# Performance work log

Measured on AMD Instinct MI355X. Metric: run time of the kernel, lower is better.

Reference implementation:

```python
import jax, jax.numpy as jnp
import numpy as np

IN_DIM = 128
OUT_DIM = 128
NUM_HEADS = 4
HEAD_DIM = OUT_DIM // NUM_HEADS
TEMP = 0.2
NEG_SLOPE = 0.2


def _xavier(key, shape, gain=1.414):
    fan_in, fan_out = shape[-2], shape[-1]
    limit = gain * np.sqrt(6.0 / (fan_in + fan_out))
    return jax.random.uniform(key, shape, jnp.float32, -limit, limit)


def setup_inputs() -> dict:
    key = jax.random.key(0)
    k_h, k_W, k_a, k_mw, k_mb = jax.random.split(key, 5)
    B, N = 4, 2048
    h = jax.random.normal(k_h, (B, N, IN_DIM), jnp.float32)
    W = _xavier(k_W, (NUM_HEADS, IN_DIM, HEAD_DIM))
    a = _xavier(k_a, (NUM_HEADS, 2 * HEAD_DIM, 1))
    merge_w = _xavier(k_mw, (OUT_DIM, OUT_DIM))  # nn.Linear weight [out, in]
    merge_b = jnp.zeros((OUT_DIM,), jnp.float32)
    return {"h": h, "W": W, "a": a, "merge_w": merge_w, "merge_b": merge_b}


def reference(h, W, a, merge_w, merge_b):
    B, N, _ = h.shape
    # Wh: [B, H, N, head_dim]
    Wh = jnp.einsum('bni,hio->bhno', h, W)
    a_sq = a[..., 0]                                  # [H, 2*hd]
    a_src, a_dst = a_sq[:, :HEAD_DIM], a_sq[:, HEAD_DIM:]
    # additive score decomposition avoids the NxNx2hd concat blowup
    s_src = jnp.einsum('bhno,ho->bhn', Wh, a_src)     # contribution of node i (row)
    s_dst = jnp.einsum('bhno,ho->bhn', Wh, a_dst)     # contribution of node j (col)
    e = s_src[:, :, :, None] + s_dst[:, :, None, :]   # [B, H, N, N]
    e = jnp.where(e > 0, e, NEG_SLOPE * e)            # LeakyReLU(0.2)
    alpha = jax.nn.softmax(e / TEMP, axis=3)          # softmax over neighbors j
    h_prime_heads = jnp.einsum('bhnm,bhmo->bhno', alpha, Wh)
    h_concat = h_prime_heads.transpose(0, 2, 1, 3).reshape(B, N, OUT_DIM)
    h_prime = h_concat @ merge_w.T + merge_b
    return h_prime, alpha.mean(axis=1)
```

## Files before the change

kernel.cpp:

```cpp
#include <hip/hip_runtime.h>
#include <stddef.h>

#define NN 2048
#define DIN 128
#define HD 32

typedef __attribute__((ext_vector_type(8))) short short8;
typedef __attribute__((ext_vector_type(4))) float f32x4;

constexpr float SLOPE = 0.2f;
constexpr float LC = 7.2134752044448170f;

__device__ __forceinline__ unsigned int pack_rne(float a, float b){
    unsigned int xa = __float_as_uint(a), xb = __float_as_uint(b);
    unsigned int ra = (xa + 0x7fffu + ((xa >> 16) & 1u)) >> 16;
    unsigned int rb = (xb + 0x7fffu + ((xb >> 16) & 1u)) >> 16;
    return ra | (rb << 16);
}

__global__ __launch_bounds__(256) void kWh(const float* __restrict__ hg,
                                           const float* __restrict__ Wg,
                                           float* __restrict__ Wh)
{
    __shared__ float Wl[DIN*HD];
    __shared__ float Hl[8][DIN+4];
    const int t = threadIdx.x;
    const int bh = blockIdx.x >> 5;
    const int tile = blockIdx.x & 31;
    const int b = bh >> 2, hh = bh & 3;
    for (int i = t; i < DIN*HD; i += 256) Wl[i] = Wg[hh*DIN*HD + i];
    const int o = t & 31, r = t >> 5;
    for (int it = 0; it < 8; ++it){
        const int nb = tile*64 + it*8;
        __syncthreads();
        {
            const float4 v = *(const float4*)&hg[((size_t)b*NN + nb + r)*DIN + o*4];
            *(float4*)&Hl[r][o*4] = v;
        }
        __syncthreads();
        float acc = 0.f;
        #pragma unroll 8
        for (int i = 0; i < DIN; ++i) acc = fmaf(Hl[r][i], Wl[i*HD+o], acc);
        Wh[((size_t)bh*NN + nb + r)*HD + o] = acc;
    }
}

__global__ __launch_bounds__(256) void kScore(const float* __restrict__ Wh,
                                              const float* __restrict__ ag,
                                              float* __restrict__ sSrc,
                                              float* __restrict__ sDst,
                                              float* __restrict__ maxPart)
{
    __shared__ float al[64];
    __shared__ float wred[4];
    const int t = threadIdx.x;
    const int bh = blockIdx.x >> 3, seg = blockIdx.x & 7;
    const int hh = bh & 3;
    if (t < 64) al[t] = ag[hh*64 + t];
    __syncthreads();
    const int n = seg*256 + t;
    const float4* wr = (const float4*)&Wh[((size_t)bh*NN + n)*HD];
    float ss = 0.f, sd = 0.f;
    #pragma unroll
    for (int q = 0; q < 8; ++q){
        float4 w = wr[q];
        ss += w.x*al[q*4+0] + w.y*al[q*4+1] + w.z*al[q*4+2] + w.w*al[q*4+3];
        sd += w.x*al[32+q*4+0] + w.y*al[32+q*4+1] + w.z*al[32+q*4+2] + w.w*al[32+q*4+3];
    }
    sSrc[bh*NN+n] = ss; sDst[bh*NN+n] = sd;
    float lmax = sd;
    #pragma unroll
    for (int off = 32; off > 0; off >>= 1) lmax = fmaxf(lmax, __shfl_down(lmax, off));
    if ((t & 63) == 0) wred[t >> 6] = lmax;
    __syncthreads();
    if (t == 0) maxPart[bh*8 + seg] = fmaxf(fmaxf(wred[0], wred[1]), fmaxf(wred[2], wred[3]));
}

__global__ __launch_bounds__(256) void kAttnM(const float* __restrict__ Wh,
                                              const float* __restrict__ sSrc,
                                              const float* __restrict__ sDst,
                                              const float* __restrict__ maxPart,
                                              float* __restrict__ invZ,
                                              unsigned short* __restrict__ hcb)
{
    __shared__ unsigned short WtT[32][136];
    __shared__ float sdl[128];
    const int t = threadIdx.x;
    const int wv = t >> 6, lane = t & 63;
    const int q = lane >> 4, c = lane & 15;
    const int bh = blockIdx.x >> 5;
    const int n0 = (blockIdx.x & 31)*64 + wv*16;
    const int b = bh >> 2, hh = bh & 3;
    float mx = maxPart[bh*8];
    #pragma unroll
    for (int i = 1; i < 8; ++i) mx = fmaxf(mx, maxPart[bh*8 + i]);
    const float ssrc = sSrc[bh*NN + n0 + c];
    const float q0 = ssrc + mx;
    const float R = fmaxf(q0, SLOPE*q0) * LC;
    const float a1 = ssrc*LC - R;
    const float a2 = SLOPE*LC*ssrc - R;
    f32x4 acc0 = {0.f,0.f,0.f,0.f}, acc1 = {0.f,0.f,0.f,0.f};
    float Zp = 0.f;
    const size_t whbase = (size_t)bh*NN*HD;
    for (int mt = 0; mt < 16; ++mt){
        const int mb = mt*128;
        __syncthreads();
        #pragma unroll
        for (int ii = 0; ii < 2; ++ii){
            const int idx = t + 256*ii;
            const int c4 = idx & 7, rp = idx >> 3;
            const float4 v0 = *(const float4*)&Wh[whbase + (size_t)(mb + 2*rp)*HD + c4*4];
            const float4 v1 = *(const float4*)&Wh[whbase + (size_t)(mb + 2*rp + 1)*HD + c4*4];
            const unsigned int* b0 = (const unsigned int*)&v0;
            const unsigned int* b1 = (const unsigned int*)&v1;
            #pragma unroll
            for (int k = 0; k < 4; ++k){
                unsigned int xa = b0[k], xb = b1[k];
                unsigned int pk = ((xa + 0x7fffu + ((xa>>16)&1u)) >> 16)
                                | (((xb + 0x7fffu + ((xb>>16)&1u)) >> 16) << 16);
                *(unsigned int*)&WtT[c4*4 + k][2*rp] = pk;
            }
        }
        if (t < 128) sdl[t] = LC * sDst[bh*NN + mb + t];
        __syncthreads();
        #pragma unroll
        for (int ks = 0; ks < 4; ++ks){
            const int m8 = ks*32 + q*8;
            float p[8];
            #pragma unroll
            for (int j = 0; j < 8; ++j){
                const float u = sdl[m8 + j];
                p[j] = exp2f(fmaxf(a1 + u, fmaf(SLOPE, u, a2)));
                Zp += p[j];
            }
            short8 aF;
            #pragma unroll
            for (int j = 0; j < 8; j += 2){
                ((unsigned int*)&aF)[j>>1] = (__float_as_uint(p[j]) >> 16)
                                           | (__float_as_uint(p[j+1]) & 0xffff0000u);
            }
            const short8 bF0 = *(const short8*)&WtT[c][m8];
            const short8 bF1 = *(const short8*)&WtT[16 + c][m8];
            acc0 = __builtin_amdgcn_mfma_f32_16x16x32_bf16(aF, bF0, acc0, 0, 0, 0);
            acc1 = __builtin_amdgcn_mfma_f32_16x16x32_bf16(aF, bF1, acc1, 0, 0, 0);
        }
    }
    Zp += __shfl_xor(Zp, 16);
    Zp += __shfl_xor(Zp, 32);
    const float iz = 1.0f / Zp;
    if (q == 0) invZ[bh*NN + n0 + c] = iz;
    #pragma unroll
    for (int reg = 0; reg < 4; ++reg){
        const int row = q*4 + reg;
        const float izr = __shfl(iz, row);
        const size_t base = ((size_t)b*NN + n0 + row)*128 + hh*32;
        hcb[base + c]      = (unsigned short)((pack_rne(acc0[reg]*izr, 0.f)) & 0xffffu);
        hcb[base + 16 + c] = (unsigned short)((pack_rne(acc1[reg]*izr, 0.f)) & 0xffffu);
    }
}

__global__ __launch_bounds__(256) void kAlpha(const float* __restrict__ sSrc,
                                              const float* __restrict__ sDst,
                                              const float* __restrict__ maxPart,
                                              const float* __restrict__ invZ,
                                              float* __restrict__ out1)
{
    __shared__ float sdl[4][NN];
    const int t = threadIdx.x;
    const int b = blockIdx.x >> 9;
    const int n0 = (blockIdx.x & 511) * 4;
    for (int i = t; i < 4*NN; i += 256)
        sdl[i >> 11][i & (NN-1)] = LC * sDst[(size_t)(b*4 + (i>>11))*NN + (i & (NN-1))];
    __syncthreads();
    float a1[4][4], a2[4][4], cf[4][4];
    #pragma unroll
    for (int hh = 0; hh < 4; ++hh){
        float mx = maxPart[(b*4+hh)*8];
        #pragma unroll
        for (int i = 1; i < 8; ++i) mx = fmaxf(mx, maxPart[(b*4+hh)*8 + i]);
        #pragma unroll
        for (int rr = 0; rr < 4; ++rr){
            const int bhn = (b*4+hh)*NN + n0 + rr;
            const float ss = sSrc[bhn];
            const float q0 = ss + mx;
            const float R = fmaxf(q0, SLOPE*q0)*LC;
            a1[rr][hh] = ss*LC - R;
            a2[rr][hh] = SLOPE*LC*ss - R;
            cf[rr][hh] = 0.25f * invZ[bhn];
        }
    }
    for (int mb = 0; mb < NN; mb += 256){
        const int m = mb + t;
        const float u0 = sdl[0][m], u1 = sdl[1][m], u2 = sdl[2][m], u3 = sdl[3][m];
        #pragma unroll
        for (int rr = 0; rr < 4; ++rr){
            float v;
            v  = cf[rr][0]*exp2f(fmaxf(a1[rr][0]+u0, fmaf(SLOPE, u0, a2[rr][0])));
            v += cf[rr][1]*exp2f(fmaxf(a1[rr][1]+u1, fmaf(SLOPE, u1, a2[rr][1])));
            v += cf[rr][2]*exp2f(fmaxf(a1[rr][2]+u2, fmaf(SLOPE, u2, a2[rr][2])));
            v += cf[rr][3]*exp2f(fmaxf(a1[rr][3]+u3, fmaf(SLOPE, u3, a2[rr][3])));
            out1[((size_t)b*NN + n0 + rr)*NN + m] = v;
        }
    }
}

__global__ __launch_bounds__(256) void kMergeM(const unsigned short* __restrict__ hcb,
                                               const float* __restrict__ mw,
                                               const float* __restrict__ mbv,
                                               float* __restrict__ out0)
{
    __shared__ unsigned short mwb[128][136];
    const int t = threadIdx.x;
    const int wv = t >> 6, lane = t & 63;
    const int q = lane >> 4, c = lane & 15;
    for (int i = t; i < 128*64; i += 256){
        const int j = i >> 6, k2 = i & 63;
        const float2 v = *(const float2*)&mw[j*128 + k2*2];
        *(unsigned int*)&mwb[j][k2*2] = pack_rne(v.x, v.y);
    }
    __syncthreads();
    const int row0 = blockIdx.x*64 + wv*16;
    f32x4 acc[8];
    #pragma unroll
    for (int ot = 0; ot < 8; ++ot) acc[ot] = (f32x4){0.f,0.f,0.f,0.f};
    #pragma unroll
    for (int ks = 0; ks < 4; ++ks){
        const short8 aF = *(const short8*)&hcb[((size_t)row0 + c)*128 + ks*32 + q*8];
        #pragma unroll
        for (int ot = 0; ot < 8; ++ot){
            const short8 bF = *(const short8*)&mwb[ot*16 + c][ks*32 + q*8];
            acc[ot] = __builtin_amdgcn_mfma_f32_16x16x32_bf16(aF, bF, acc[ot], 0, 0, 0);
        }
    }
    #pragma unroll
    for (int ot = 0; ot < 8; ++ot){
        const int col = ot*16 + c;
        const float bias = mbv[col];
        #pragma unroll
        for (int reg = 0; reg < 4; ++reg){
            const size_t row = (size_t)row0 + q*4 + reg;
            out0[row*128 + col] = acc[ot][reg] + bias;
        }
    }
}

extern "C" void kernel_launch(void* const* d_in, const int* in_sizes, int n_in,
                              void* d_out, int out_size, void* d_ws, size_t ws_size,
                              hipStream_t stream)
{
    const float* hg  = (const float*)d_in[0];
    const float* Wg  = (const float*)d_in[1];
    const float* ag  = (const float*)d_in[2];
    const float* mw  = (const float*)d_in[3];
    const float* mbv = (const float*)d_in[4];
    float* out0 = (float*)d_out;
    float* out1 = out0 + (size_t)4*NN*128;

    float* ws     = (float*)d_ws;
    float* Wh     = ws;
    float* sSrc   = Wh + 1048576;
    float* sDst   = sSrc + 32768;
    float* maxPart= sDst + 32768;
    float* invZ   = maxPart + 128;
    unsigned short* hcb = (unsigned short*)(invZ + 32768);

    hipLaunchKernelGGL(kWh,    dim3(512),  dim3(256), 0, stream, hg, Wg, Wh);
    hipLaunchKernelGGL(kScore, dim3(128),  dim3(256), 0, stream, Wh, ag, sSrc, sDst, maxPart);
    hipLaunchKernelGGL(kAttnM, dim3(512),  dim3(256), 0, stream, Wh, sSrc, sDst, maxPart, invZ, hcb);
    hipLaunchKernelGGL(kAlpha, dim3(2048), dim3(256), 0, stream, sSrc, sDst, maxPart, invZ, out1);
    hipLaunchKernelGGL(kMergeM,dim3(128),  dim3(256), 0, stream, hcb, mw, mbv, out0);
}
```

Measured before the change: 169.3 us.

## Fuse Wh projection with score computation and emit transposed bf16 Wh

```diff
diff --git a/kernel.cpp b/kernel.cpp
--- a/kernel.cpp
+++ b/kernel.cpp
@@ -18,68 +18,110 @@
     return ra | (rb << 16);
 }
 
-__global__ __launch_bounds__(256) void kWh(const float* __restrict__ hg,
-                                           const float* __restrict__ Wg,
-                                           float* __restrict__ Wh)
-{
-    __shared__ float Wl[DIN*HD];
-    __shared__ float Hl[8][DIN+4];
-    const int t = threadIdx.x;
-    const int bh = blockIdx.x >> 5;
-    const int tile = blockIdx.x & 31;
-    const int b = bh >> 2, hh = bh & 3;
-    for (int i = t; i < DIN*HD; i += 256) Wl[i] = Wg[hh*DIN*HD + i];
-    const int o = t & 31, r = t >> 5;
-    for (int it = 0; it < 8; ++it){
-        const int nb = tile*64 + it*8;
-        __syncthreads();
-        {
-            const float4 v = *(const float4*)&hg[((size_t)b*NN + nb + r)*DIN + o*4];
-            *(float4*)&Hl[r][o*4] = v;
-        }
-        __syncthreads();
-        float acc = 0.f;
-        #pragma unroll 8
-        for (int i = 0; i < DIN; ++i) acc = fmaf(Hl[r][i], Wl[i*HD+o], acc);
-        Wh[((size_t)bh*NN + nb + r)*HD + o] = acc;
-    }
-}
-
-__global__ __launch_bounds__(256) void kScore(const float* __restrict__ Wh,
-                                              const float* __restrict__ ag,
-                                              float* __restrict__ sSrc,
-                                              float* __restrict__ sDst,
-                                              float* __restrict__ maxPart)
-{
-    __shared__ float al[64];
-    __shared__ float wred[4];
-    const int t = threadIdx.x;
-    const int bh = blockIdx.x >> 3, seg = blockIdx.x & 7;
-    const int hh = bh & 3;
-    if (t < 64) al[t] = ag[hh*64 + t];
+__global__ __launch_bounds__(256) void kWhScore(const float* __restrict__ hg,
+                                                const float* __restrict__ Wg,
+                                                const float* __restrict__ ag,
+                                                unsigned short* __restrict__ whT,
+                                                float* __restrict__ sSrc,
+                                                float* __restrict__ sDst,
+                                                float* __restrict__ maxPart)
+{
+    __shared__ float Hl[32][132];
+    __shared__ float wal[8][128];
+    __shared__ float al[256];
+    const int t = threadIdx.x;
+    const int b = blockIdx.x >> 6;
+    const int tile = blockIdx.x & 63;
+    const int n0 = tile*32;
+    #pragma unroll
+    for (int ii = 0; ii < 4; ++ii){
+        const int idx = t + 256*ii;
+        const int r = idx >> 5, c4 = idx & 31;
+        *(float4*)&Hl[r][c4*4] = *(const float4*)&hg[((size_t)b*NN + n0 + r)*DIN + c4*4];
+    }
+    al[t] = ag[t];
     __syncthreads();
-    const int n = seg*256 + t;
-    const float4* wr = (const float4*)&Wh[((size_t)bh*NN + n)*HD];
-    float ss = 0.f, sd = 0.f;
-    #pragma unroll
-    for (int q = 0; q < 8; ++q){
-        float4 w = wr[q];
-        ss += w.x*al[q*4+0] + w.y*al[q*4+1] + w.z*al[q*4+2] + w.w*al[q*4+3];
-        sd += w.x*al[32+q*4+0] + w.y*al[32+q*4+1] + w.z*al[32+q*4+2] + w.w*al[32+q*4+3];
-    }
-    sSrc[bh*NN+n] = ss; sDst[bh*NN+n] = sd;
-    float lmax = sd;
-    #pragma unroll
-    for (int off = 32; off > 0; off >>= 1) lmax = fmaxf(lmax, __shfl_down(lmax, off));
-    if ((t & 63) == 0) wred[t >> 6] = lmax;
+    #pragma unroll
+    for (int jj = 0; jj < 4; ++jj){
+        const int idx = t + 256*jj;
+        const int combo = idx >> 7, i = idx & 127;
+        const int hh = combo >> 1, d = combo & 1;
+        const float* wrow = &Wg[hh*4096 + i*32];
+        const float* av = &al[hh*64 + d*32];
+        float s = 0.f;
+        #pragma unroll
+        for (int q = 0; q < 8; ++q){
+            const float4 w = *(const float4*)&wrow[q*4];
+            s += w.x*av[q*4] + w.y*av[q*4+1] + w.z*av[q*4+2] + w.w*av[q*4+3];
+        }
+        wal[combo][i] = s;
+    }
     __syncthreads();
-    if (t == 0) maxPart[bh*8 + seg] = fmaxf(fmaxf(wred[0], wred[1]), fmaxf(wred[2], wred[3]));
-}
-
-__global__ __launch_bounds__(256) void kAttnM(const float* __restrict__ Wh,
+    {
+        const int combo = t >> 5, nl = t & 31;
+        const int hh = combo >> 1, d = combo & 1;
+        float s = 0.f;
+        #pragma unroll
+        for (int q = 0; q < 32; ++q){
+            const float4 hv = *(const float4*)&Hl[nl][q*4];
+            const float4 wv = *(const float4*)&wal[combo][q*4];
+            s += hv.x*wv.x + hv.y*wv.y + hv.z*wv.z + hv.w*wv.w;
+        }
+        const int bh = b*4 + hh;
+        if (d == 0) sSrc[bh*NN + n0 + nl] = s;
+        else {
+            sDst[bh*NN + n0 + nl] = s;
+            float lm = s;
+            #pragma unroll
+            for (int off = 1; off < 32; off <<= 1) lm = fmaxf(lm, __shfl_xor(lm, off));
+            if (nl == 0) maxPart[bh*64 + tile] = lm;
+        }
+    }
+    const int og = t >> 5, nl = t & 31;
+    const int o0 = og*4;
+    float acc[16];
+    #pragma unroll
+    for (int k = 0; k < 16; ++k) acc[k] = 0.f;
+    for (int kc = 0; kc < 16; ++kc){
+        const float4 hA = *(const float4*)&Hl[nl][kc*8];
+        const float4 hB = *(const float4*)&Hl[nl][kc*8+4];
+        const float hreg[8] = {hA.x,hA.y,hA.z,hA.w,hB.x,hB.y,hB.z,hB.w};
+        #pragma unroll
+        for (int hh = 0; hh < 4; ++hh){
+            #pragma unroll
+            for (int i8 = 0; i8 < 8; ++i8){
+                const float4 w = *(const float4*)&Wg[hh*4096 + (kc*8+i8)*32 + o0];
+                acc[hh*4+0] = fmaf(hreg[i8], w.x, acc[hh*4+0]);
+                acc[hh*4+1] = fmaf(hreg[i8], w.y, acc[hh*4+1]);
+                acc[hh*4+2] = fmaf(hreg[i8], w.z, acc[hh*4+2]);
+                acc[hh*4+3] = fmaf(hreg[i8], w.w, acc[hh*4+3]);
+            }
+        }
+    }
+    #pragma unroll
+    for (int hh = 0; hh < 4; ++hh){
+        #pragma unroll
+        for (int j = 0; j < 4; ++j){
+            const unsigned int x = __float_as_uint(acc[hh*4+j]);
+            whT[((size_t)(b*4+hh)*32 + o0 + j)*NN + n0 + nl] =
+                (unsigned short)((x + 0x7fffu + ((x>>16)&1u)) >> 16);
+        }
+    }
+}
+
+__global__ void kMaxR(const float* __restrict__ maxPart, float* __restrict__ maxFull){
+    const int t = threadIdx.x;
+    if (t < 16){
+        float m = maxPart[t*64];
+        for (int i = 1; i < 64; ++i) m = fmaxf(m, maxPart[t*64+i]);
+        maxFull[t] = m;
+    }
+}
+
+__global__ __launch_bounds__(256) void kAttnM(const unsigned short* __restrict__ whT,
                                               const float* __restrict__ sSrc,
                                               const float* __restrict__ sDst,
-                                              const float* __restrict__ maxPart,
+                                              const float* __restrict__ maxFull,
                                               float* __restrict__ invZ,
                                               unsigned short* __restrict__ hcb)
 {
@@ -91,9 +133,7 @@
     const int bh = blockIdx.x >> 5;
     const int n0 = (blockIdx.x & 31)*64 + wv*16;
     const int b = bh >> 2, hh = bh & 3;
-    float mx = maxPart[bh*8];
-    #pragma unroll
-    for (int i = 1; i < 8; ++i) mx = fmaxf(mx, maxPart[bh*8 + i]);
+    const float mx = maxFull[bh];
     const float ssrc = sSrc[bh*NN + n0 + c];
     const float q0 = ssrc + mx;
     const float R = fmaxf(q0, SLOPE*q0) * LC;
@@ -101,25 +141,14 @@
     const float a2 = SLOPE*LC*ssrc - R;
     f32x4 acc0 = {0.f,0.f,0.f,0.f}, acc1 = {0.f,0.f,0.f,0.f};
     float Zp = 0.f;
-    const size_t whbase = (size_t)bh*NN*HD;
     for (int mt = 0; mt < 16; ++mt){
         const int mb = mt*128;
         __syncthreads();
         #pragma unroll
-        for (int ii = 0; ii < 2; ++ii){
-            const int idx = t + 256*ii;
-            const int c4 = idx & 7, rp = idx >> 3;
-            const float4 v0 = *(const float4*)&Wh[whbase + (size_t)(mb + 2*rp)*HD + c4*4];
-            const float4 v1 = *(const float4*)&Wh[whbase + (size_t)(mb + 2*rp + 1)*HD + c4*4];
-            const unsigned int* b0 = (const unsigned int*)&v0;
-            const unsigned int* b1 = (const unsigned int*)&v1;
-            #pragma unroll
-            for (int k = 0; k < 4; ++k){
-                unsigned int xa = b0[k], xb = b1[k];
-                unsigned int pk = ((xa + 0x7fffu + ((xa>>16)&1u)) >> 16)
-                                | (((xb + 0x7fffu + ((xb>>16)&1u)) >> 16) << 16);
-                *(unsigned int*)&WtT[c4*4 + k][2*rp] = pk;
-            }
+        for (int ps = 0; ps < 2; ++ps){
+            const int o = ps*16 + (t >> 4);
+            const int mo = (t & 15)*8;
+            *(short8*)&WtT[o][mo] = *(const short8*)&whT[((size_t)bh*32 + o)*NN + mb + mo];
         }
         if (t < 128) sdl[t] = LC * sDst[bh*NN + mb + t];
         __syncthreads();
@@ -161,7 +190,7 @@
 
 __global__ __launch_bounds__(256) void kAlpha(const float* __restrict__ sSrc,
                                               const float* __restrict__ sDst,
-                                              const float* __restrict__ maxPart,
+                                              const float* __restrict__ maxFull,
                                               const float* __restrict__ invZ,
                                               float* __restrict__ out1)
 {
@@ -175,9 +204,7 @@
     float a1[4][4], a2[4][4], cf[4][4];
     #pragma unroll
     for (int hh = 0; hh < 4; ++hh){
-        float mx = maxPart[(b*4+hh)*8];
-        #pragma unroll
-        for (int i = 1; i < 8; ++i) mx = fmaxf(mx, maxPart[(b*4+hh)*8 + i]);
+        const float mx = maxFull[b*4+hh];
         #pragma unroll
         for (int rr = 0; rr < 4; ++rr){
             const int bhn = (b*4+hh)*NN + n0 + rr;
@@ -256,17 +283,18 @@
     float* out0 = (float*)d_out;
     float* out1 = out0 + (size_t)4*NN*128;
 
-    float* ws     = (float*)d_ws;
-    float* Wh     = ws;
-    float* sSrc   = Wh + 1048576;
-    float* sDst   = sSrc + 32768;
-    float* maxPart= sDst + 32768;
-    float* invZ   = maxPart + 128;
-    unsigned short* hcb = (unsigned short*)(invZ + 32768);
-
-    hipLaunchKernelGGL(kWh,    dim3(512),  dim3(256), 0, stream, hg, Wg, Wh);
-    hipLaunchKernelGGL(kScore, dim3(128),  dim3(256), 0, stream, Wh, ag, sSrc, sDst, maxPart);
-    hipLaunchKernelGGL(kAttnM, dim3(512),  dim3(256), 0, stream, Wh, sSrc, sDst, maxPart, invZ, hcb);
-    hipLaunchKernelGGL(kAlpha, dim3(2048), dim3(256), 0, stream, sSrc, sDst, maxPart, invZ, out1);
-    hipLaunchKernelGGL(kMergeM,dim3(128),  dim3(256), 0, stream, hcb, mw, mbv, out0);
-}
+    float* ws      = (float*)d_ws;
+    float* sSrc    = ws;
+    float* sDst    = sSrc + 32768;
+    float* maxPart = sDst + 32768;
+    float* maxFull = maxPart + 1024;
+    float* invZ    = maxFull + 16;
+    unsigned short* whT = (unsigned short*)(invZ + 32768);
+    unsigned short* hcb = whT + (size_t)16*32*NN;
+
+    hipLaunchKernelGGL(kWhScore, dim3(256),  dim3(256), 0, stream, hg, Wg, ag, whT, sSrc, sDst, maxPart);
+    hipLaunchKernelGGL(kMaxR,    dim3(1),    dim3(64),  0, stream, maxPart, maxFull);
+    hipLaunchKernelGGL(kAttnM,   dim3(512),  dim3(256), 0, stream, whT, sSrc, sDst, maxFull, invZ, hcb);
+    hipLaunchKernelGGL(kAlpha,   dim3(2048), dim3(256), 0, stream, sSrc, sDst, maxFull, invZ, out1);
+    hipLaunchKernelGGL(kMergeM,  dim3(128),  dim3(256), 0, stream, hcb, mw, mbv, out0);
+}
```

After: 169.5 us. No clear change (+0.1%).
